# Kernel tuning notes

Measured on AMD Instinct MI355X. Metric: run time of the kernel, lower is better.

## Reference

```python
import jax, jax.numpy as jnp
import numpy as np

GATE_THRESH = 0.4
ALPHA_FN = lambda L: 1.0 - 1.0 / L  # length-adaptive alpha, called with actual L
EPS_NORM = 1e-12  # F.normalize eps
EPS_LN = 1e-5     # LayerNorm eps


def setup_inputs() -> dict:
    key = jax.random.key(0)
    B, L, H, V = 64, 2048, 128, 32000
    ks = jax.random.split(key, 8)
    s = lambda k, shape, fan: jax.random.normal(k, shape, jnp.float32) * (1.0 / np.sqrt(fan))
    return {
        "seq": jax.random.randint(ks[0], (B, L), 0, V, dtype=jnp.int64),
        "embed_w": jax.random.normal(ks[1], (V, H), jnp.float32) * 0.02,
        "ff_w1": s(ks[2], (2 * H, H), H), "ff_b1": jnp.zeros((2 * H,), jnp.float32),
        "ff_w2": s(ks[3], (H, 2 * H), 2 * H), "ff_b2": jnp.zeros((H,), jnp.float32),
        "ln_g": jnp.ones((H,), jnp.float32), "ln_b": jnp.zeros((H,), jnp.float32),
        "kp_w": s(ks[4], (H, H), H),
        "rp_w": s(ks[5], (H, H), H), "rp_b": jnp.zeros((H,), jnp.float32),
        "out_w": s(ks[6], (V, H), H), "out_b": jnpp if False else jnp.zeros((V,), jnp.float32),
    }


def reference(seq, embed_w, ff_w1, ff_b1, ff_w2, ff_b2, ln_g, ln_b, kp_w, rp_w, rp_b, out_w, out_b):
    h = embed_w[seq]                                            # [B,L,H]
    ff = jnp.maximum(h @ ff_w1.T + ff_b1, 0.0) @ ff_w2.T + ff_b2
    x = h + ff
    mu = x.mean(-1, keepdims=True)
    var = x.var(-1, keepdims=True)                              # biased, as LayerNorm
    h = (x - mu) / jnp.sqrt(var + EPS_LN) * ln_g + ln_b
    B, L, H = h.shape
    alpha = ALPHA_FN(L)
    k_all = jnp.einsum('blh,oh->blo', h, kp_w)                  # kp has no bias

    def step(M, k):                                             # M:[B,H,H], k:[B,H]
        kn = k / jnp.maximum(jnp.linalg.norm(k, axis=-1, keepdims=True), EPS_NORM)
        vp = jnp.einsum('bij,bj->bi', M, kn)
        d = k - vp
        delta = d[:, :, None] * kn[:, None, :]                  # outer product [B,H,H]
        fire = (jnp.linalg.norm(d, axis=-1) >= GATE_THRESH * jnp.linalg.norm(k, axis=-1)).astype(k.dtype)
        return M + (1.0 - alpha) * fire[:, None, None] * delta, None

    M0 = jnp.zeros((B, H, H), h.dtype)
    M, _ = jax.lax.scan(step, M0, jnp.swapaxes(k_all[:, :-1, :], 0, 1))  # scan over L-1 steps
    q = k_all[:, -1, :]
    read = jnp.einsum('bij,bj->bi', M, q)
    return (read @ rp_w.T + rp_b) @ out_w.T + out_b             # [B,V]
```

## Files before the change

kernel.cpp:

```cpp
#include <hip/hip_runtime.h>
#include <hip/hip_bf16.h>
#include <stdint.h>

#define Bn 64
#define Ln 2048
#define Hn 128
#define Vn 32000
#define THn 256
#define LAMBDA_ (1.0f/2048.0f)
#define CC 32
#define NCH (Ln/CC)
#define KP  132
#define VS  132
#define VPW (CC*VS)
#define ADS 131
#define ADW (CC*ADS+4)
#define GS  36
#define GXS 33
#define MSR 36
#define MSW 576
#define HS  132

typedef short bf16x8 __attribute__((ext_vector_type(8)));
typedef float f32x4  __attribute__((ext_vector_type(4)));

__device__ __forceinline__ float rdlane(float v, int s) {
  return __int_as_float(__builtin_amdgcn_readlane(__float_as_int(v), s));
}

template <int CTRL>
__device__ __forceinline__ float dpp_add(float x) {
  int t = __builtin_amdgcn_update_dpp(0, __float_as_int(x), CTRL, 0xf, 0xf, false);
  return x + __int_as_float(t);
}
__device__ __forceinline__ float wave_sum64(float x) {
  x = dpp_add<0x111>(x);
  x = dpp_add<0x112>(x);
  x = dpp_add<0x114>(x);
  x = dpp_add<0x118>(x);
  x = dpp_add<0x142>(x);
  x = dpp_add<0x143>(x);
  return rdlane(x, 63);
}

__device__ __forceinline__ uint32_t packhl(float x) {
  uint32_t bx = __float_as_uint(x);
  float hf = __uint_as_float(bx & 0xFFFF0000u);
  uint32_t bl = __float_as_uint(x - hf);
  return (bx >> 16) | (bl & 0xFFFF0000u);
}
__device__ __forceinline__ float unpackhl(uint32_t u) {
  return __uint_as_float(u << 16) + __uint_as_float(u & 0xFFFF0000u);
}

struct FragHL { bf16x8 h; bf16x8 l; };
__device__ __forceinline__ FragHL mkfrag(const uint32_t* u) {
  union { uint32_t a[4]; bf16x8 v; } H, L;
  H.a[0] = __builtin_amdgcn_perm(u[1], u[0], 0x05040100u);
  H.a[1] = __builtin_amdgcn_perm(u[3], u[2], 0x05040100u);
  H.a[2] = __builtin_amdgcn_perm(u[5], u[4], 0x05040100u);
  H.a[3] = __builtin_amdgcn_perm(u[7], u[6], 0x05040100u);
  L.a[0] = __builtin_amdgcn_perm(u[1], u[0], 0x07060302u);
  L.a[1] = __builtin_amdgcn_perm(u[3], u[2], 0x07060302u);
  L.a[2] = __builtin_amdgcn_perm(u[5], u[4], 0x07060302u);
  L.a[3] = __builtin_amdgcn_perm(u[7], u[6], 0x07060302u);
  FragHL f; f.h = H.v; f.l = L.v; return f;
}

__device__ __forceinline__ void ld8(const uint32_t* p, uint32_t* u) {
  const uint4 a = *reinterpret_cast<const uint4*>(p);
  const uint4 b = *reinterpret_cast<const uint4*>(p + 4);
  u[0]=a.x; u[1]=a.y; u[2]=a.z; u[3]=a.w;
  u[4]=b.x; u[5]=b.y; u[6]=b.z; u[7]=b.w;
}

__device__ __forceinline__ bf16x8 asbf(uint4 u) {
  union { uint4 a; bf16x8 v; } c; c.a = u; return c.v;
}

__device__ __forceinline__ f32x4 mfma16(bf16x8 a, bf16x8 b, f32x4 c) {
  return __builtin_amdgcn_mfma_f32_16x16x32_bf16(a, b, c, 0, 0, 0);
}

__device__ __forceinline__ void gload_lds4(const uint32_t* g, uint32_t* l) {
  __builtin_amdgcn_global_load_lds(
      (const __attribute__((address_space(1))) void*)g,
      (__attribute__((address_space(3))) void*)l, 4, 0, 0);
}

__global__ __launch_bounds__(256) void p0_pack(
    const float* __restrict__ w1, const float* __restrict__ w2,
    const float* __restrict__ kp, uint32_t* __restrict__ wp)
{
  const int id = blockIdx.x*256 + threadIdx.x;
  const float* src; uint32_t *dh, *dl; int p;
  if (id < 16384)      { src = w1; p = id;         dh = wp;         dl = wp+16384; }
  else if (id < 32768) { src = w2; p = id-16384;   dh = wp+32768;   dl = wp+49152; }
  else                 { src = kp; p = id-32768;   dh = wp+65536;   dl = wp+73728; }
  const float x0 = src[2*p], x1 = src[2*p+1];
  const uint32_t b0 = __float_as_uint(x0), b1 = __float_as_uint(x1);
  const float l0f = x0 - __uint_as_float(b0 & 0xFFFF0000u);
  const float l1f = x1 - __uint_as_float(b1 & 0xFFFF0000u);
  dh[p] = (b0 >> 16) | ((b1 >> 16) << 16);
  dl[p] = (__float_as_uint(l0f) >> 16) | ((__float_as_uint(l1f) >> 16) << 16);
}

__global__ __launch_bounds__(256, 2) void p1_fused(
    const int* __restrict__ seq,
    const float* __restrict__ embed_w,
    const uint32_t* __restrict__ wp,
    const float* __restrict__ ff_b1, const float* __restrict__ ff_b2,
    const float* __restrict__ ln_g, const float* __restrict__ ln_b,
    uint32_t* __restrict__ knp_all, float* __restrict__ norm_all)
{
  __shared__ __align__(16) uint32_t h_p[64*HS];
  __shared__ __align__(16) uint32_t u_p[64*HS];
  __shared__ float part1[256], part2[256];
  __shared__ float mul[64], rsl[64];
  __shared__ int sid[64];

  const int tid  = threadIdx.x;
  const int lane = tid & 63;
  const int w    = __builtin_amdgcn_readfirstlane(tid >> 6);
  const int q4   = lane >> 4;
  const int m16  = lane & 15;
  const int tile0 = blockIdx.x * 64;

  const uint32_t* w1h = wp;
  const uint32_t* w1l = wp + 16384;
  const uint32_t* w2h = wp + 32768;
  const uint32_t* w2l = wp + 49152;
  const uint32_t* kph = wp + 65536;
  const uint32_t* kpl = wp + 73728;

  if (tid < 64) sid[tid] = seq[tile0 + tid];
  __syncthreads();

  {
    const int t = tid >> 2, part = tid & 3;
    const float4* erow =
        reinterpret_cast<const float4*>(embed_w + (size_t)sid[t]*Hn) + part*8;
    #pragma unroll
    for (int c = 0; c < 8; ++c) {
      float4 v = erow[c];
      int j = part*32 + c*4;
      h_p[t*HS+j+0] = packhl(v.x); h_p[t*HS+j+1] = packhl(v.y);
      h_p[t*HS+j+2] = packhl(v.z); h_p[t*HS+j+3] = packhl(v.w);
    }
  }
  __syncthreads();

  f32x4 acc2[4][2];
  #pragma unroll
  for (int tt=0;tt<4;++tt)
    #pragma unroll
    for (int ct=0;ct<2;++ct) acc2[tt][ct] = (f32x4){0.f,0.f,0.f,0.f};

  #pragma unroll 1
  for (int ho=0; ho<2; ++ho) {
    #pragma unroll 1
    for (int tt=0; tt<4; ++tt) {
      FragHL fa[4];
      #pragma unroll
      for (int kk=0;kk<4;++kk) {
        uint32_t ua[8];
        ld8(&h_p[(16*tt+m16)*HS + 32*kk + 8*q4], ua);
        fa[kk] = mkfrag(ua);
      }
      #pragma unroll
      for (int ct=0; ct<2; ++ct) {
        const int ob = 128*ho + 32*w + 16*ct;
        f32x4 a = (f32x4){0.f,0.f,0.f,0.f};
        #pragma unroll
        for (int kk=0;kk<4;++kk) {
          const size_t wi = (size_t)(ob+m16)*64 + 16*kk + 4*q4;
          bf16x8 bh = asbf(*reinterpret_cast<const uint4*>(&w1h[wi]));
          bf16x8 bl = asbf(*reinterpret_cast<const uint4*>(&w1l[wi]));
          a = mfma16(fa[kk].h, bh, a);
          a = mfma16(fa[kk].h, bl, a);
          a = mfma16(fa[kk].l, bh, a);
        }
        const float bb = ff_b1[ob + m16];
        #pragma unroll
        for (int reg=0;reg<4;++reg) {
          float uv = fmaxf(a[reg] + bb, 0.f);
          u_p[(16*tt+4*q4+reg)*HS + 32*w + 16*ct + m16] = packhl(uv);
        }
      }
    }
    __syncthreads();
    #pragma unroll 1
    for (int tt=0; tt<4; ++tt) {
      FragHL fu[4];
      #pragma unroll
      for (int kk=0;kk<4;++kk) {
        uint32_t ua[8];
        ld8(&u_p[(16*tt+m16)*HS + 32*kk + 8*q4], ua);
        fu[kk] = mkfrag(ua);
      }
      #pragma unroll
      for (int ct=0; ct<2; ++ct) {
        const int ib = 32*w + 16*ct;
        f32x4 a = acc2[tt][ct];
        #pragma unroll
        for (int kk=0;kk<4;++kk) {
          const size_t wi = (size_t)(ib+m16)*128 + 64*ho + 16*kk + 4*q4;
          bf16x8 bh = asbf(*reinterpret_cast<const uint4*>(&w2h[wi]));
          bf16x8 bl = asbf(*reinterpret_cast<const uint4*>(&w2l[wi]));
          a = mfma16(fu[kk].h, bh, a);
          a = mfma16(fu[kk].h, bl, a);
          a = mfma16(fu[kk].l, bh, a);
        }
        acc2[tt][ct] = a;
      }
    }
    __syncthreads();
  }

  float xx[4][2][4];
  #pragma unroll
  for (int tt=0;tt<4;++tt)
    #pragma unroll
    for (int ct=0;ct<2;++ct) {
      const int col = 32*w + 16*ct + m16;
      const float b2 = ff_b2[col];
      #pragma unroll
      for (int reg=0;reg<4;++reg) {
        const float hval = unpackhl(h_p[(16*tt+4*q4+reg)*HS + col]);
        xx[tt][ct][reg] = acc2[tt][ct][reg] + b2 + hval;
      }
    }
  #pragma unroll
  for (int tt=0;tt<4;++tt)
    #pragma unroll
    for (int reg=0;reg<4;++reg) {
      float s1 = xx[tt][0][reg] + xx[tt][1][reg];
      float s2 = xx[tt][0][reg]*xx[tt][0][reg] + xx[tt][1][reg]*xx[tt][1][reg];
      s1 += __shfl_xor(s1,1); s1 += __shfl_xor(s1,2);
      s1 += __shfl_xor(s1,4); s1 += __shfl_xor(s1,8);
      s2 += __shfl_xor(s2,1); s2 += __shfl_xor(s2,2);
      s2 += __shfl_xor(s2,4); s2 += __shfl_xor(s2,8);
      if (m16==0) {
        part1[w*64 + 16*tt+4*q4+reg] = s1;
        part2[w*64 + 16*tt+4*q4+reg] = s2;
      }
    }
  __syncthreads();
  if (tid < 64) {
    const float mu = (part1[tid]+part1[64+tid]+part1[128+tid]+part1[192+tid])*(1.0f/128.0f);
    const float ms = (part2[tid]+part2[64+tid]+part2[128+tid]+part2[192+tid])*(1.0f/128.0f);
    mul[tid] = mu;
    rsl[tid] = rsqrtf(ms - mu*mu + 1e-5f);
  }
  __syncthreads();

  #pragma unroll
  for (int tt=0;tt<4;++tt)
    #pragma unroll
    for (int ct=0;ct<2;++ct) {
      const int col = 32*w + 16*ct + m16;
      const float g = ln_g[col], bb = ln_b[col];
      #pragma unroll
      for (int reg=0;reg<4;++reg) {
        const int tok = 16*tt+4*q4+reg;
        const float hn = (xx[tt][ct][reg] - mul[tok])*rsl[tok]*g + bb;
        h_p[tok*HS + col] = packhl(hn);
      }
    }
  __syncthreads();

  f32x4 ak[4][2];
  #pragma unroll 1
  for (int tt=0;tt<4;++tt) {
    FragHL fh[4];
    #pragma unroll
    for (int kk=0;kk<4;++kk) {
      uint32_t ua[8];
      ld8(&h_p[(16*tt+m16)*HS + 32*kk + 8*q4], ua);
      fh[kk] = mkfrag(ua);
    }
    #pragma unroll
    for (int ct=0;ct<2;++ct) {
      const int ob = 32*w + 16*ct;
      f32x4 a = (f32x4){0.f,0.f,0.f,0.f};
      #pragma unroll
      for (int kk=0;kk<4;++kk) {
        const size_t wi = (size_t)(ob+m16)*64 + 16*kk + 4*q4;
        bf16x8 bh = asbf(*reinterpret_cast<const uint4*>(&kph[wi]));
        bf16x8 bl = asbf(*reinterpret_cast<const uint4*>(&kpl[wi]));
        a = mfma16(fh[kk].h, bh, a);
        a = mfma16(fh[kk].h, bl, a);
        a = mfma16(fh[kk].l, bh, a);
      }
      ak[tt][ct] = a;
    }
  }
  #pragma unroll
  for (int tt=0;tt<4;++tt)
    #pragma unroll
    for (int reg=0;reg<4;++reg) {
      float s = ak[tt][0][reg]*ak[tt][0][reg] + ak[tt][1][reg]*ak[tt][1][reg];
      s += __shfl_xor(s,1); s += __shfl_xor(s,2);
      s += __shfl_xor(s,4); s += __shfl_xor(s,8);
      if (m16==0) part1[w*64 + 16*tt+4*q4+reg] = s;
    }
  __syncthreads();
  if (tid < 64) {
    const float nn = part1[tid]+part1[64+tid]+part1[128+tid]+part1[192+tid];
    const float nrm = sqrtf(nn);
    norm_all[tile0 + tid] = nrm;
    mul[tid] = 1.0f / fmaxf(nrm, 1e-12f);
  }
  __syncthreads();
  #pragma unroll
  for (int tt=0;tt<4;++tt)
    #pragma unroll
    for (int ct=0;ct<2;++ct) {
      const int col = 32*w + 16*ct + m16;
      #pragma unroll
      for (int reg=0;reg<4;++reg) {
        const int tok = 16*tt+4*q4+reg;
        knp_all[(size_t)(tile0+tok)*Hn + col] = packhl(ak[tt][ct][reg]*mul[tok]);
      }
    }
}

__global__ __launch_bounds__(768, 3) void p2_scan(
    const uint32_t* __restrict__ knp_all, const float* __restrict__ norm_all,
    float* __restrict__ read_ws)
{
  const int tid  = threadIdx.x;
  const int lane = tid & 63;
  const int wv   = __builtin_amdgcn_readfirstlane(tid >> 6);
  const int q    = lane >> 4;
  const int m    = lane & 15;
  const int b    = blockIdx.x;

  __shared__ __align__(16) uint32_t kn_p[3*CC*KP];
  __shared__ __align__(16) float    vp0L[2*VPW];
  __shared__ __align__(16) float    adL [2*ADW];
  __shared__ __align__(16) float    Gt  [2*CC*GS];
  __shared__ __align__(16) float    GxT [CC*GXS];
  __shared__ __align__(16) uint32_t msc [8*MSW];
  __shared__ float nrm_l[3*CC];

  const uint32_t* knb = knp_all + (size_t)b*Ln*Hn;
  const float*    nb  = norm_all + (size_t)b*Ln;

  const int swm  = ((m>>3)&3)<<3;
  const int swm2 = (((16+m)>>3)&3)<<3;

  {
    if (tid < 256) {
      const int t = tid>>3, g = tid&7;
      const int sw = ((t>>3)&3)<<3;
      const uint4* src = reinterpret_cast<const uint4*>(knb + t*Hn + g*16);
      uint32_t* dstb = &kn_p[t*KP];
      *reinterpret_cast<uint4*>(&dstb[(16*g+0) ^ sw])  = src[0];
      *reinterpret_cast<uint4*>(&dstb[(16*g+4) ^ sw])  = src[1];
      *reinterpret_cast<uint4*>(&dstb[(16*g+8) ^ sw])  = src[2];
      *reinterpret_cast<uint4*>(&dstb[(16*g+12) ^ sw]) = src[3];
    } else if (tid < 512) {
      const int idx = tid-256, t = idx>>3, g = idx&7;
      const int sw = ((t>>3)&3)<<3;
      const uint4* src = reinterpret_cast<const uint4*>(knb + CC*Hn + t*Hn + g*16);
      uint32_t* dstb = &kn_p[CC*KP + t*KP];
      *reinterpret_cast<uint4*>(&dstb[(16*g+0) ^ sw])  = src[0];
      *reinterpret_cast<uint4*>(&dstb[(16*g+4) ^ sw])  = src[1];
      *reinterpret_cast<uint4*>(&dstb[(16*g+8) ^ sw])  = src[2];
      *reinterpret_cast<uint4*>(&dstb[(16*g+12) ^ sw]) = src[3];
    } else if (tid < 512+2*CC) {
      nrm_l[tid-512] = nb[tid-512];
    }
  }
  __syncthreads();

  {
    if (wv >= 9) {
      const int gi = wv - 9;
      if (gi < 3) {
        const int ti = (gi==2) ? 1 : 0;
        const int si = (gi==0) ? 0 : 1;
        const int ra = 16*ti+m, rb = 16*si+m;
        const int swa = ((ra>>3)&3)<<3, swb = ((rb>>3)&3)<<3;
        f32x4 g4 = (f32x4){0.f,0.f,0.f,0.f};
        #pragma unroll
        for (int kk=0; kk<4; ++kk) {
          uint32_t ua[8], ub[8];
          ld8(&kn_p[ra*KP + ((32*kk + 8*q) ^ swa)], ua);
          ld8(&kn_p[rb*KP + ((32*kk + 8*q) ^ swb)], ub);
          FragHL fa = mkfrag(ua), fb = mkfrag(ub);
          g4 = mfma16(fa.h, fb.h, g4);
          g4 = mfma16(fa.h, fb.l, g4);
          g4 = mfma16(fa.l, fb.h, g4);
        }
        #pragma unroll
        for (int reg=0; reg<4; ++reg)
          Gt[(16*ti + 4*q + reg)*GS + 16*si + m] = g4[reg];
        if (gi==1) {
          #pragma unroll
          for (int reg=0; reg<4; ++reg)
            Gt[(16*si + m)*GS + 16*ti + 4*q + reg] = g4[reg];
        }
      }
    }
    if (wv >= 1 && wv <= 8) {
      const int h0 = 16*(wv-1);
      const float nr0 = nrm_l[m], nr1 = nrm_l[16+m];
      const uint4 r0 = *reinterpret_cast<const uint4*>(&kn_p[m*KP + ((h0 + 4*q) ^ swm)]);
      const uint4 r1 = *reinterpret_cast<const uint4*>(&kn_p[(16+m)*KP + ((h0 + 4*q) ^ swm2)]);
      const uint32_t* pr0 = &r0.x; const uint32_t* pr1 = &r1.x;
      #pragma unroll
      for (int reg=0; reg<4; ++reg) {
        const int h = h0 + 4*q + reg;
        vp0L[m*VS + h]      = nr0*unpackhl(pr0[reg]);
        vp0L[(16+m)*VS + h] = nr1*unpackhl(pr1[reg]);
      }
    }
  }
  __syncthreads();

  if (wv == 0) {
    #pragma unroll 1
    for (int ch=0; ch<NCH; ++ch) {
      const int cur = ch%3;
      const int sel = ch & 1;
      const uint32_t* knc = &kn_p[cur*CC*KP];

      float ad0[CC], ad1[CC];
      float* adW = &adL[sel*ADW];
      const float* vpR = &vp0L[sel*VPW];
      const float* GtS = &Gt[sel*CC*GS];
      const int lid = lane & 31;
      const float nrmv = nrm_l[cur*CC + lid];
      float grt = GtS[0*GS + lid];
      float grn = GtS[1*GS + lid];
      __builtin_amdgcn_s_setprio(1);
      #pragma unroll
      for (int t=0;t<CC;++t) {
        float grn2 = 0.f;
        if (t+2 < CC) grn2 = GtS[(t+2)*GS + lid];
        float a0c0 = vpR[t*VS + lane];
        float a1c0 = vpR[t*VS + 64 + lane];
        float a0c1=0.f, a0c2=0.f, a0c3=0.f;
        float a1c1=0.f, a1c2=0.f, a1c3=0.f;
        #pragma unroll
        for (int s=0; s<t; ++s) {
          const float g = rdlane(grt, s);
          switch (s & 3) {
            case 0: a0c0 -= g*ad0[s]; a1c0 -= g*ad1[s]; break;
            case 1: a0c1 -= g*ad0[s]; a1c1 -= g*ad1[s]; break;
            case 2: a0c2 -= g*ad0[s]; a1c2 -= g*ad1[s]; break;
            default:a0c3 -= g*ad0[s]; a1c3 -= g*ad1[s]; break;
          }
        }
        const float acc0 = (a0c0+a0c1)+(a0c2+a0c3);
        const float acc1 = (a1c0+a1c1)+(a1c2+a1c3);
        const float sqt = wave_sum64(acc0*acc0 + acc1*acc1);
        const float nrm = rdlane(nrmv, t);
        if (ch==NCH-1 && t==CC-1) {
          const int swt = ((t>>3)&3)<<3;
          const float kn0 = unpackhl(knc[t*KP + (lane ^ swt)]);
          const float kn1 = unpackhl(knc[t*KP + ((64+lane) ^ swt)]);
          read_ws[b*Hn + lane]      = nrm*(nrm*kn0 - acc0);
          read_ws[b*Hn + 64 + lane] = nrm*(nrm*kn1 - acc1);
        } else {
          const float at = (sqt >= 0.16f*nrm*nrm) ? LAMBDA_ : 0.f;
          ad0[t] = at*acc0; ad1[t] = at*acc1;
          adW[t*ADS + lane]      = ad0[t];
          adW[t*ADS + 64 + lane] = ad1[t];
        }
        grt = grn; grn = grn2;
      }
      __builtin_amdgcn_s_setprio(0);

      __syncthreads();
      if (ch==NCH-1) break;
      __syncthreads();
    }
  } else if (wv <= 8) {
    f32x4 Macc[8];
    #pragma unroll
    for (int ct=0; ct<8; ++ct) Macc[ct] = (f32x4){0.f,0.f,0.f,0.f};
    const int h0 = 16*(wv-1);

    #pragma unroll 1
    for (int ch=0; ch<NCH; ++ch) {
      const int cur = ch%3, nx1 = (ch+1)%3, nx2 = (ch+2)%3;
      const int sel = ch & 1;
      const uint32_t* knc = &kn_p[cur*CC*KP];
      const uint32_t* knN = &kn_p[nx1*CC*KP];
      const uint32_t* knP = &kn_p[nx2*CC*KP];
      const bool havn  = (ch+1 < NCH);
      const bool havn2 = (ch+2 < NCH);
      (void)knc;

      float pfn = 0.f;
      if (havn2 && tid >= 288 && tid < 320) pfn = nb[(ch+2)*CC + (tid-288)];

      if (havn) {
        if (ch >= 1) {
          const float* adR = &adL[(1-sel)*ADW];
          uint32_t ap[8];
          #pragma unroll
          for (int j=0;j<8;++j)
            ap[j] = packhl(adR[(8*q+j)*ADS + h0 + m]);
          FragHL fa = mkfrag(ap);
          #pragma unroll
          for (int ct=0; ct<8; ++ct) {
            uint32_t bu[8];
            #pragma unroll
            for (int j=0;j<8;++j)
              bu[j] = knP[(8*q+j)*KP + ((16*ct+m) ^ (q<<3))];
            FragHL fb = mkfrag(bu);
            Macc[ct] = mfma16(fa.h, fb.h, Macc[ct]);
            Macc[ct] = mfma16(fa.h, fb.l, Macc[ct]);
            Macc[ct] = mfma16(fa.l, fb.h, Macc[ct]);
          }
        }
        {
          f32x4 v0 = (f32x4){0.f,0.f,0.f,0.f};
          f32x4 v1 = (f32x4){0.f,0.f,0.f,0.f};
          uint32_t* mybase = &msc[(wv-1)*MSW];
          #pragma unroll
          for (int kk=0; kk<4; ++kk) {
            #pragma unroll
            for (int c2=0; c2<2; ++c2) {
              const int ct = 2*kk + c2;
              #pragma unroll
              for (int reg=0; reg<4; ++reg)
                mybase[(4*q+reg)*MSR + 16*c2 + m] = packhl(Macc[ct][reg]);
            }
            uint32_t ua[8], ub[8];
            ld8(&mybase[m*MSR + 8*q], ua);
            FragHL fa = mkfrag(ua);
            ld8(&knN[m*KP + ((32*kk + 8*q) ^ swm)], ub);
            FragHL fb = mkfrag(ub);
            v0 = mfma16(fa.h, fb.h, v0);
            v0 = mfma16(fa.h, fb.l, v0);
            v0 = mfma16(fa.l, fb.h, v0);
            ld8(&knN[(16+m)*KP + ((32*kk + 8*q) ^ swm2)], ub);
            fb = mkfrag(ub);
            v1 = mfma16(fa.h, fb.h, v1);
            v1 = mfma16(fa.h, fb.l, v1);
            v1 = mfma16(fa.l, fb.h, v1);
          }
          float* vpW = &vp0L[(1-sel)*VPW];
          const float nr0 = nrm_l[nx1*CC + m];
          const float nr1 = nrm_l[nx1*CC + 16 + m];
          const uint4 r0 = *reinterpret_cast<const uint4*>(&knN[m*KP + ((h0 + 4*q) ^ swm)]);
          const uint4 r1 = *reinterpret_cast<const uint4*>(&knN[(16+m)*KP + ((h0 + 4*q) ^ swm2)]);
          const uint32_t* pr0 = &r0.x; const uint32_t* pr1 = &r1.x;
          #pragma unroll
          for (int reg=0; reg<4; ++reg) {
            const int h = h0 + 4*q + reg;
            vpW[m*VS + h]      = nr0*unpackhl(pr0[reg]) - v0[reg];
            vpW[(16+m)*VS + h] = nr1*unpackhl(pr1[reg]) - v1[reg];
          }
        }
      }

      __syncthreads();
      if (ch==NCH-1) break;

      {
        f32x4 c0 = (f32x4){0.f,0.f,0.f,0.f};
        f32x4 c1 = (f32x4){0.f,0.f,0.f,0.f};
        {
          const float* adR = &adL[sel*ADW];
          uint32_t* mybase = &msc[(wv-1)*MSW];
          #pragma unroll
          for (int c2=0; c2<2; ++c2)
            #pragma unroll
            for (int reg=0; reg<4; ++reg)
              mybase[(4*q+reg)*MSR + 16*c2 + m] =
                  packhl(adR[(16*c2+m)*ADS + h0 + 4*q + reg]);
          uint32_t ua[8], gb[8];
          ld8(&mybase[m*MSR + 8*q], ua);
          FragHL fa = mkfrag(ua);
          #pragma unroll
          for (int jj=0;jj<8;++jj) gb[jj] = packhl(GxT[m*GXS + 8*q + jj]);
          FragHL fb = mkfrag(gb);
          c0 = mfma16(fa.h, fb.h, c0);
          c0 = mfma16(fa.h, fb.l, c0);
          c0 = mfma16(fa.l, fb.h, c0);
          #pragma unroll
          for (int jj=0;jj<8;++jj) gb[jj] = packhl(GxT[(16+m)*GXS + 8*q + jj]);
          fb = mkfrag(gb);
          c1 = mfma16(fa.h, fb.h, c1);
          c1 = mfma16(fa.h, fb.l, c1);
          c1 = mfma16(fa.l, fb.h, c1);
        }
        {
          float* vpW = &vp0L[(1-sel)*VPW];
          #pragma unroll
          for (int reg=0; reg<4; ++reg) {
            const int h = h0 + 4*q + reg;
            vpW[m*VS + h]      -= c0[reg];
            vpW[(16+m)*VS + h] -= c1[reg];
          }
        }
        if (havn2) {
          const uint32_t* gsrc = knb + (size_t)(ch+2)*CC*Hn;
          uint32_t* ldst = &kn_p[nx2*CC*KP];
          #pragma unroll
          for (int r=0; r<4; ++r) {
            const int t = (wv-1)*4 + r;
            const int sw = ((t>>3)&3)<<3;
            #pragma unroll
            for (int half=0; half<2; ++half) {
              gload_lds4(gsrc + t*Hn + ((half*64 + lane) ^ sw),
                         &ldst[t*KP + half*64]);
            }
          }
          if (tid >= 288 && tid < 320) nrm_l[nx2*CC + (tid-288)] = pfn;
        }
      }
      __syncthreads();
    }
  } else if (wv <= 10) {
    const int tj = wv - 9;
    #pragma unroll 1
    for (int ch=0; ch<NCH; ++ch) {
      const int cur = ch%3, nx1 = (ch+1)%3;
      const uint32_t* knc = &kn_p[cur*CC*KP];
      const uint32_t* knN = &kn_p[nx1*CC*KP];
      const bool havn = (ch+1 < NCH);

      if (havn) {
        #pragma unroll
        for (int ts=0; ts<2; ++ts) {
          const int ra = 16*tj+m, rb = 16*ts+m;
          const int swa = ((ra>>3)&3)<<3, swb = ((rb>>3)&3)<<3;
          f32x4 g4 = (f32x4){0.f,0.f,0.f,0.f};
          #pragma unroll
          for (int kk=0; kk<4; ++kk) {
            uint32_t ua[8], ub[8];
            ld8(&knN[ra*KP + ((32*kk + 8*q) ^ swa)], ua);
            ld8(&knc[rb*KP + ((32*kk + 8*q) ^ swb)], ub);
            FragHL fa = mkfrag(ua), fb = mkfrag(ub);
            g4 = mfma16(fa.h, fb.h, g4);
            g4 = mfma16(fa.h, fb.l, g4);
            g4 = mfma16(fa.l, fb.h, g4);
          }
          #pragma unroll
          for (int reg=0; reg<4; ++reg)
            GxT[(16*tj + 4*q + reg)*GXS + 16*ts + m] = g4[reg];
        }
      }
      __syncthreads();
      if (ch==NCH-1) break;
      __syncthreads();
    }
  } else {
    #pragma unroll 1
    for (int ch=0; ch<NCH; ++ch) {
      const int nx1 = (ch+1)%3;
      const int sel = ch & 1;
      const uint32_t* knN = &kn_p[nx1*CC*KP];
      const bool havn = (ch+1 < NCH);

      if (havn) {
        #pragma unroll
        for (int gi=0; gi<3; ++gi) {
          const int ti = (gi==2) ? 1 : 0;
          const int si = (gi==0) ? 0 : 1;
          const int ra = 16*ti+m, rb = 16*si+m;
          const int swa = ((ra>>3)&3)<<3, swb = ((rb>>3)&3)<<3;
          f32x4 g4 = (f32x4){0.f,0.f,0.f,0.f};
          #pragma unroll
          for (int kk=0; kk<4; ++kk) {
            uint32_t ua[8], ub[8];
            ld8(&knN[ra*KP + ((32*kk + 8*q) ^ swa)], ua);
            ld8(&knN[rb*KP + ((32*kk + 8*q) ^ swb)], ub);
            FragHL fa = mkfrag(ua), fb = mkfrag(ub);
            g4 = mfma16(fa.h, fb.h, g4);
            g4 = mfma16(fa.h, fb.l, g4);
            g4 = mfma16(fa.l, fb.h, g4);
          }
          float* GtW = &Gt[(1-sel)*CC*GS];
          #pragma unroll
          for (int reg=0; reg<4; ++reg)
            GtW[(16*ti + 4*q + reg)*GS + 16*si + m] = g4[reg];
          if (gi==1) {
            #pragma unroll
            for (int reg=0; reg<4; ++reg)
              GtW[(16*si + m)*GS + 16*ti + 4*q + reg] = g4[reg];
          }
        }
      }
      __syncthreads();
      if (ch==NCH-1) break;
      __syncthreads();
    }
  }
}

__global__ __launch_bounds__(128) void p3a(
    const float* __restrict__ read_ws, const float* __restrict__ rp_w,
    const float* __restrict__ rp_b, float* __restrict__ o1_ws)
{
  __shared__ float rd[128];
  const int b = blockIdx.x, t = threadIdx.x;
  rd[t] = read_ws[b*Hn + t];
  __syncthreads();
  float acc = rp_b[t];
  const float* wr = rp_w + t*Hn;
  #pragma unroll 4
  for (int i = 0; i < Hn; ++i) acc += rd[i]*wr[i];
  o1_ws[b*Hn + t] = acc;
}

__global__ __launch_bounds__(256) void p3b(
    const float* __restrict__ o1_ws, const float* __restrict__ out_w,
    const float* __restrict__ out_b, float* __restrict__ out)
{
  __shared__ __align__(16) float o1[8192];
  const int tid = threadIdx.x;
  #pragma unroll
  for (int c = 0; c < 32; ++c) o1[c*256+tid] = o1_ws[c*256+tid];
  __syncthreads();
  const int v = blockIdx.x*256 + tid;
  float acc[64];
  const float ob = out_b[v];
  #pragma unroll
  for (int bb = 0; bb < 64; ++bb) acc[bb] = ob;
  const float4* wrow = reinterpret_cast<const float4*>(out_w + (size_t)v*Hn);
  #pragma unroll 1
  for (int r4 = 0; r4 < 32; ++r4) {
    const float4 wv = wrow[r4];
    #pragma unroll
    for (int bb = 0; bb < 64; ++bb) {
      const float4 ov = *reinterpret_cast<const float4*>(&o1[bb*Hn + r4*4]);
      acc[bb] += wv.x*ov.x + wv.y*ov.y + wv.z*ov.z + wv.w*ov.w;
    }
  }
  #pragma unroll
  for (int bb = 0; bb < 64; ++bb) out[(size_t)bb*Vn + v] = acc[bb];
}

extern "C" void kernel_launch(void* const* d_in, const int* in_sizes, int n_in,
                              void* d_out, int out_size, void* d_ws, size_t ws_size,
                              hipStream_t stream)
{
  const int*   seq     = (const int*)  d_in[0];
  const float* embed_w = (const float*)d_in[1];
  const float* ff_w1   = (const float*)d_in[2];
  const float* ff_b1   = (const float*)d_in[3];
  const float* ff_w2   = (const float*)d_in[4];
  const float* ff_b2   = (const float*)d_in[5];
  const float* ln_g    = (const float*)d_in[6];
  const float* ln_b    = (const float*)d_in[7];
  const float* kp_w    = (const float*)d_in[8];
  const float* rp_w    = (const float*)d_in[9];
  const float* rp_b    = (const float*)d_in[10];
  const float* out_w   = (const float*)d_in[11];
  const float* out_b   = (const float*)d_in[12];

  float* ws          = (float*)d_ws;
  uint32_t* knp_all  = (uint32_t*)ws;
  float* norm_all    = ws + (size_t)Bn*Ln*Hn;
  float* read_ws     = norm_all + (size_t)Bn*Ln;
  float* o1_ws       = read_ws + Bn*Hn;
  uint32_t* wp       = (uint32_t*)(o1_ws + Bn*Hn);

  p0_pack<<<dim3(160), dim3(256), 0, stream>>>(ff_w1, ff_w2, kp_w, wp);
  p1_fused<<<dim3(2048), dim3(256), 0, stream>>>(
      seq, embed_w, wp, ff_b1, ff_b2, ln_g, ln_b, knp_all, norm_all);
  p2_scan<<<dim3(64), dim3(768), 0, stream>>>(knp_all, norm_all, read_ws);
  p3a<<<dim3(64), dim3(128), 0, stream>>>(read_ws, rp_w, rp_b, o1_ws);
  p3b<<<dim3(125), dim3(256), 0, stream>>>(o1_ws, out_w, out_b, (float*)d_out);
}
```

Baseline: 700.8 us.

## Stage transposed key chunk in LDS and shrink key ring to double buffer

The M-update MFMA previously read B fragments from the row-major key buffer with eight strided scalar LDS loads per tile. It now reads one vectorised ld8 per tile from a transposed, swizzled copy (knT). The M-update warps fill that copy each chunk from global memory, using the current chunk's keys for the update in the next iteration. The three-slot key ring becomes two slots, the prefetch reuses the freed slot, and the norm ring grows to four slots to keep lifetimes valid. This adds a global read and a transposed LDS write per chunk and changes buffer lifetimes across the barriers.

```diff
diff --git a/kernel.cpp b/kernel.cpp
--- a/kernel.cpp
+++ b/kernel.cpp
@@ -11,6 +11,7 @@
 #define CC 32
 #define NCH (Ln/CC)
 #define KP  132
+#define KTS 36
 #define VS  132
 #define VPW (CC*VS)
 #define ADS 131
@@ -336,13 +337,14 @@
   const int m    = lane & 15;
   const int b    = blockIdx.x;
 
-  __shared__ __align__(16) uint32_t kn_p[3*CC*KP];
+  __shared__ __align__(16) uint32_t kn_p[2*CC*KP];
+  __shared__ __align__(16) uint32_t knT [128*KTS];
   __shared__ __align__(16) float    vp0L[2*VPW];
   __shared__ __align__(16) float    adL [2*ADW];
   __shared__ __align__(16) float    Gt  [2*CC*GS];
   __shared__ __align__(16) float    GxT [CC*GXS];
   __shared__ __align__(16) uint32_t msc [8*MSW];
-  __shared__ float nrm_l[3*CC];
+  __shared__ float nrm_l[4*CC];
 
   const uint32_t* knb = knp_all + (size_t)b*Ln*Hn;
   const float*    nb  = norm_all + (size_t)b*Ln;
@@ -423,7 +425,7 @@
   if (wv == 0) {
     #pragma unroll 1
     for (int ch=0; ch<NCH; ++ch) {
-      const int cur = ch%3;
+      const int cur = ch&1;
       const int sel = ch & 1;
       const uint32_t* knc = &kn_p[cur*CC*KP];
 
@@ -432,7 +434,7 @@
       const float* vpR = &vp0L[sel*VPW];
       const float* GtS = &Gt[sel*CC*GS];
       const int lid = lane & 31;
-      const float nrmv = nrm_l[cur*CC + lid];
+      const float nrmv = nrm_l[(ch&3)*CC + lid];
       float grt = GtS[0*GS + lid];
       float grn = GtS[1*GS + lid];
       __builtin_amdgcn_s_setprio(1);
@@ -486,14 +488,11 @@
 
     #pragma unroll 1
     for (int ch=0; ch<NCH; ++ch) {
-      const int cur = ch%3, nx1 = (ch+1)%3, nx2 = (ch+2)%3;
+      const int cur = ch&1, nx1 = (ch+1)&1;
       const int sel = ch & 1;
-      const uint32_t* knc = &kn_p[cur*CC*KP];
       const uint32_t* knN = &kn_p[nx1*CC*KP];
-      const uint32_t* knP = &kn_p[nx2*CC*KP];
       const bool havn  = (ch+1 < NCH);
       const bool havn2 = (ch+2 < NCH);
-      (void)knc;
 
       float pfn = 0.f;
       if (havn2 && tid >= 288 && tid < 320) pfn = nb[(ch+2)*CC + (tid-288)];
@@ -508,10 +507,10 @@
           FragHL fa = mkfrag(ap);
           #pragma unroll
           for (int ct=0; ct<8; ++ct) {
+            const int hcol = 16*ct + m;
+            const int swz = ((hcol>>3)&3)<<3;
             uint32_t bu[8];
-            #pragma unroll
-            for (int j=0;j<8;++j)
-              bu[j] = knP[(8*q+j)*KP + ((16*ct+m) ^ (q<<3))];
+            ld8(&knT[hcol*KTS + (8*q ^ swz)], bu);
             FragHL fb = mkfrag(bu);
             Macc[ct] = mfma16(fa.h, fb.h, Macc[ct]);
             Macc[ct] = mfma16(fa.h, fb.l, Macc[ct]);
@@ -546,8 +545,8 @@
             v1 = mfma16(fa.l, fb.h, v1);
           }
           float* vpW = &vp0L[(1-sel)*VPW];
-          const float nr0 = nrm_l[nx1*CC + m];
-          const float nr1 = nrm_l[nx1*CC + 16 + m];
+          const float nr0 = nrm_l[((ch+1)&3)*CC + m];
+          const float nr1 = nrm_l[((ch+1)&3)*CC + 16 + m];
           const uint4 r0 = *reinterpret_cast<const uint4*>(&knN[m*KP + ((h0 + 4*q) ^ swm)]);
           const uint4 r1 = *reinterpret_cast<const uint4*>(&knN[(16+m)*KP + ((h0 + 4*q) ^ swm2)]);
           const uint32_t* pr0 = &r0.x; const uint32_t* pr1 = &r1.x;
@@ -564,6 +563,14 @@
       if (ch==NCH-1) break;
 
       {
+        uint2 tv[4];
+        #pragma unroll
+        for (int r=0; r<4; ++r) {
+          const int t = (wv-1)*4 + r;
+          tv[r] = *reinterpret_cast<const uint2*>(
+              &knb[(size_t)ch*CC*Hn + t*Hn + 2*lane]);
+        }
+
         f32x4 c0 = (f32x4){0.f,0.f,0.f,0.f};
         f32x4 c1 = (f32x4){0.f,0.f,0.f,0.f};
         {
@@ -600,9 +607,19 @@
             vpW[(16+m)*VS + h] -= c1[reg];
           }
         }
+        {
+          const int h2 = 2*lane;
+          const int swz = ((h2>>3)&3)<<3;
+          #pragma unroll
+          for (int r=0; r<4; ++r) {
+            const int t = (wv-1)*4 + r;
+            knT[h2*KTS     + (t ^ swz)] = tv[r].x;
+            knT[(h2+1)*KTS + (t ^ swz)] = tv[r].y;
+          }
+        }
         if (havn2) {
           const uint32_t* gsrc = knb + (size_t)(ch+2)*CC*Hn;
-          uint32_t* ldst = &kn_p[nx2*CC*KP];
+          uint32_t* ldst = &kn_p[cur*CC*KP];
           #pragma unroll
           for (int r=0; r<4; ++r) {
             const int t = (wv-1)*4 + r;
@@ -613,7 +630,7 @@
                          &ldst[t*KP + half*64]);
             }
           }
-          if (tid >= 288 && tid < 320) nrm_l[nx2*CC + (tid-288)] = pfn;
+          if (tid >= 288 && tid < 320) nrm_l[((ch+2)&3)*CC + (tid-288)] = pfn;
         }
       }
       __syncthreads();
@@ -622,7 +639,7 @@
     const int tj = wv - 9;
     #pragma unroll 1
     for (int ch=0; ch<NCH; ++ch) {
-      const int cur = ch%3, nx1 = (ch+1)%3;
+      const int cur = ch&1, nx1 = (ch+1)&1;
       const uint32_t* knc = &kn_p[cur*CC*KP];
       const uint32_t* knN = &kn_p[nx1*CC*KP];
       const bool havn = (ch+1 < NCH);
@@ -655,7 +672,7 @@
   } else {
     #pragma unroll 1
     for (int ch=0; ch<NCH; ++ch) {
-      const int nx1 = (ch+1)%3;
+      const int nx1 = (ch+1)&1;
       const int sel = ch & 1;
       const uint32_t* knN = &kn_p[nx1*CC*KP];
       const bool havn = (ch+1 < NCH);
```

After: 695.2 us. About the same (-0.8%).
